# Kernel optimization log

Measured on AMD Instinct MI355X. Metric: run time of the kernel, lower is better.

## Reference

```python
import jax, jax.numpy as jnp
import numpy as np

N = 50000          # number of graph nodes
R = 4              # number of relation types (rt_num)
E = 800000         # edges per relation (avg degree 16)
D_IN = 128
D_OUT = 64
EPS = 1e-12        # torch F.normalize eps


def setup_inputs() -> dict:
    key = jax.random.key(0)
    k1, k2, k3, k4, k5 = jax.random.split(key, 5)
    x = jax.random.normal(k1, (N, D_IN), dtype=jnp.float32)
    W = jax.random.normal(k2, (R, D_IN, D_OUT), dtype=jnp.float32)
    b = jnp.zeros((R, D_OUT), dtype=jnp.float32)
    adj_vals = jax.random.uniform(k3, (R, E), dtype=jnp.float32)
    adj_rows = jax.random.randint(k4, (R, E), 0, N, dtype=jnp.int32)
    adj_cols = jax.random.randint(k5, (R, E), 0, N, dtype=jnp.int32)
    return {"x": x, "W": W, "b": b, "adj_vals": adj_vals,
            "adj_rows": adj_rows, "adj_cols": adj_cols, "dropout": 0}


def reference(x, W, b, adj_vals, adj_rows, adj_cols, dropout):
    # dropout == 0 -> F.dropout is the identity; reference is deterministic.
    # Per-relation dense projection: xw[r] = x @ W[r]   -> [R, N, D_OUT]
    xw = jnp.einsum('nd,rdo->rno', x, W)

    def per_relation(xw_r, rows_r, cols_r, vals_r, b_r):
        # sparse adjacency SpMM: out[i] = sum_e vals[e] * xw[cols[e]] for rows[e]==i
        msg = xw_r[cols_r] * vals_r[:, None]                  # [E, D_OUT] gather
        agg = jax.ops.segment_sum(msg, rows_r, num_segments=N)  # [N, D_OUT] scatter-add
        return jax.nn.relu(agg + b_r)                          # bias + act

    outs = jax.vmap(per_relation)(xw, adj_rows, adj_cols, adj_vals, b)  # [R, N, D_OUT]
    total = jnp.sum(outs, axis=0)                               # cross-relation sum
    # L2 normalize over feature dim (torch F.normalize, dim=1)
    norm = jnp.maximum(jnp.linalg.norm(total, axis=1, keepdims=True), EPS)
    return total / norm
```

## Files before the change

### kernel.cpp

```cpp
#include <hip/hip_runtime.h>
#include <hip/hip_bf16.h>
#include <stdint.h>

#define NN 50000
#define DI 128
#define DO 64
#define NE 800000
#define NR 4
#define NB 782
#define NBUCK (NR*NB)
#define PCHUNK 7168
#define PWG ((NE + PCHUNK - 1) / PCHUNK)
#define RSCAP 4096

typedef short short8 __attribute__((ext_vector_type(8)));
typedef float f32x4  __attribute__((ext_vector_type(4)));
union FragU { uint4 u; short8 s; };

__device__ __forceinline__ uint32_t bfb(float f)
{
    __hip_bfloat16 h = __float2bfloat16(f);
    return (uint32_t)*reinterpret_cast<unsigned short*>(&h);
}

template<int N, int PER, int BLK>
__device__ inline void block_exscan(int* a)
{
    __shared__ int wsum[BLK / 64];
    int tid = threadIdx.x;
    int base = tid * PER;
    int v[PER]; int s = 0;
    #pragma unroll
    for (int j = 0; j < PER; ++j) {
        int idx = base + j;
        int x = (idx < N) ? a[idx] : 0;
        v[j] = s; s += x;
    }
    int lane = tid & 63, wv = tid >> 6;
    int inc = s;
    #pragma unroll
    for (int off = 1; off < 64; off <<= 1) {
        int u = __shfl_up(inc, off);
        if (lane >= off) inc += u;
    }
    if (lane == 63) wsum[wv] = inc;
    __syncthreads();
    int woff = 0;
    for (int w = 0; w < wv; ++w) woff += wsum[w];
    int tb = woff + inc - s;
    #pragma unroll
    for (int j = 0; j < PER; ++j) {
        int idx = base + j;
        if (idx < N) a[idx] = tb + v[j];
    }
}

__global__ __launch_bounds__(256) void convx_kernel(
    const float* __restrict__ x, uint2* __restrict__ xb)
{
    int i = blockIdx.x * 256 + threadIdx.x;
    int stride = gridDim.x * 256;
    const int total = NN * DI / 4;
    const float4* x4 = (const float4*)x;
    for (; i < total; i += stride) {
        float4 v = x4[i];
        uint2 o;
        o.x = bfb(v.x) | (bfb(v.y) << 16);
        o.y = bfb(v.z) | (bfb(v.w) << 16);
        xb[i] = o;
    }
}

__global__ __launch_bounds__(256) void wtrans_kernel(
    const float* __restrict__ W, uint16_t* __restrict__ wt)
{
    int i = blockIdx.x * 256 + threadIdx.x;
    if (i >= NR * DI * DO) return;
    int r = i >> 13;
    int k = (i >> 6) & 127;
    int n = i & 63;
    wt[((size_t)(r * DO + n) << 7) + k] = (uint16_t)bfb(W[i]);
}

__global__ __launch_bounds__(256) void gemm_mfma_kernel(
    const uint4* __restrict__ xb4, const uint4* __restrict__ wt4,
    uint16_t* __restrict__ xwb)
{
    int tid = threadIdx.x;
    int wv = __builtin_amdgcn_readfirstlane(tid >> 6);
    int lane = tid & 63;
    int n0 = blockIdx.x * 64 + wv * 16;
    if (n0 >= NN) return;
    int m16 = lane & 15, g = lane >> 4;

    FragU a[4];
    #pragma unroll
    for (int ks = 0; ks < 4; ++ks)
        a[ks].u = xb4[(size_t)(n0 + m16) * 16 + ks * 4 + g];

    #pragma unroll
    for (int r = 0; r < NR; ++r) {
        #pragma unroll
        for (int ct = 0; ct < 4; ++ct) {
            f32x4 acc = {0.f, 0.f, 0.f, 0.f};
            #pragma unroll
            for (int ks = 0; ks < 4; ++ks) {
                FragU b;
                b.u = wt4[(size_t)((r * DO + ct * 16 + m16) * 16) + ks * 4 + g];
                acc = __builtin_amdgcn_mfma_f32_16x16x32_bf16(
                    a[ks].s, b.s, acc, 0, 0, 0);
            }
            #pragma unroll
            for (int j = 0; j < 4; ++j) {
                int m = g * 4 + j;
                xwb[((size_t)r * NN + n0 + m) * 64 + ct * 16 + m16] =
                    (uint16_t)bfb(acc[j]);
            }
        }
    }
}

__global__ __launch_bounds__(256) void gemm_kernel(
    const float* __restrict__ x, const float* __restrict__ W,
    __hip_bfloat16* __restrict__ xwb)
{
    __shared__ float Wl[DI * DO];
    for (int i = threadIdx.x; i < DI * DO; i += 256) Wl[i] = W[i];
    __syncthreads();

    int wv   = __builtin_amdgcn_readfirstlane((int)(threadIdx.x >> 6));
    int lane = threadIdx.x & 63;
    int n0   = blockIdx.x * 32 + wv * 8;
    if (n0 >= NN) return;
    int nrows = NN - n0; if (nrows > 8) nrows = 8;

    if (nrows == 8) {
        const float* xr = x + (size_t)n0 * DI;
        float acc[8] = {0.f,0.f,0.f,0.f,0.f,0.f,0.f,0.f};
        #pragma unroll 8
        for (int k = 0; k < DI; ++k) {
            float w = Wl[k * DO + lane];
            #pragma unroll
            for (int rr = 0; rr < 8; ++rr)
                acc[rr] = fmaf(xr[(size_t)rr * DI + k], w, acc[rr]);
        }
        #pragma unroll
        for (int rr = 0; rr < 8; ++rr)
            xwb[(size_t)(n0 + rr) * DO + lane] = __float2bfloat16(acc[rr]);
    } else {
        for (int rr = 0; rr < nrows; ++rr) {
            const float* xr = x + (size_t)(n0 + rr) * DI;
            float acc = 0.f;
            for (int k = 0; k < DI; ++k)
                acc = fmaf(xr[k], Wl[k * DO + lane], acc);
            xwb[(size_t)(n0 + rr) * DO + lane] = __float2bfloat16(acc);
        }
    }
}

__global__ __launch_bounds__(256) void bhist_kernel(
    const int* __restrict__ rows, int* __restrict__ gtot)
{
    __shared__ int h[NB];
    int r = blockIdx.y;
    int tid = threadIdx.x;
    for (int i = tid; i < NB; i += 256) h[i] = 0;
    __syncthreads();
    const int4* rr4 = (const int4*)(rows + (size_t)r * NE);
    for (int k = blockIdx.x * 256 + tid; k < NE / 4; k += gridDim.x * 256) {
        int4 v = rr4[k];
        atomicAdd(&h[v.x >> 6], 1);
        atomicAdd(&h[v.y >> 6], 1);
        atomicAdd(&h[v.z >> 6], 1);
        atomicAdd(&h[v.w >> 6], 1);
    }
    __syncthreads();
    int* gt = gtot + r * NB;
    for (int i = tid; i < NB; i += 256)
        if (h[i]) atomicAdd(&gt[i], h[i]);
}

__global__ __launch_bounds__(512) void bases_kernel(
    const int* __restrict__ gtot, int* __restrict__ gstart,
    int* __restrict__ gcur)
{
    __shared__ int a[NBUCK + 1];
    int tid = threadIdx.x;
    for (int i = tid; i < NBUCK + 1; i += 512) a[i] = (i < NBUCK) ? gtot[i] : 0;
    __syncthreads();
    block_exscan<NBUCK + 1, 7, 512>(a);
    __syncthreads();
    for (int i = tid; i < NBUCK + 1; i += 512) {
        gstart[i] = a[i];
        if (i < NBUCK) gcur[i] = a[i];
    }
}

__global__ __launch_bounds__(512) void place_kernel(
    const int* __restrict__ rows, const int* __restrict__ cols,
    const float* __restrict__ vals, int* __restrict__ gcur,
    int2* __restrict__ csr)
{
    __shared__ int lofs[NB + 1];
    __shared__ int gbase[NB];
    __shared__ int2 stag[PCHUNK];
    int r = blockIdx.y;
    int tid = threadIdx.x;
    int e0 = blockIdx.x * PCHUNK;
    int cnt = NE - e0; if (cnt > PCHUNK) cnt = PCHUNK;
    const int*   rr = rows + (size_t)r * NE + e0;
    const int*   cc = cols + (size_t)r * NE + e0;
    const float* vv = vals + (size_t)r * NE + e0;

    for (int i = tid; i <= NB; i += 512) lofs[i] = 0;
    __syncthreads();
    for (int k = tid; k < cnt; k += 512) atomicAdd(&lofs[rr[k] >> 6], 1);
    __syncthreads();
    block_exscan<NB + 1, 2, 512>(lofs);
    __syncthreads();
    for (int b = tid; b < NB; b += 512) {
        int c = lofs[b + 1] - lofs[b];
        if (c > 0) gbase[b] = atomicAdd(&gcur[r * NB + b], c);
    }
    __syncthreads();
    for (int k = tid; k < cnt; k += 512) {
        int row = rr[k];
        int b = row >> 6;
        int slot = atomicAdd(&lofs[b], 1);
        stag[slot] = make_int2((cc[k] & 0xFFFF) | ((row & 63) << 16) | (b << 22),
                               __float_as_int(vv[k]));
    }
    __syncthreads();
    for (int i = tid; i < cnt; i += 512) {
        int2 t = stag[i];
        unsigned b2 = ((unsigned)t.x) >> 22;
        int start = b2 ? lofs[b2 - 1] : 0;
        csr[gbase[b2] + (i - start)] = t;
    }
}

__global__ __launch_bounds__(256) void rowsort_kernel(
    int2* __restrict__ csr, const int* __restrict__ gstart,
    int* __restrict__ rowptr)
{
    __shared__ int2 stag[RSCAP];
    __shared__ int cnt[64];
    __shared__ int ofs[64];
    int blk = blockIdx.x;
    int r   = blockIdx.y;
    int b   = r * NB + blk;
    int s = gstart[b], e = gstart[b + 1];
    int cntE = e - s; if (cntE > RSCAP) cntE = RSCAP;
    int tid = threadIdx.x;
    if (tid < 64) cnt[tid] = 0;
    __syncthreads();

    int2 ed[RSCAP / 256];
    #pragma unroll
    for (int j = 0; j < RSCAP / 256; ++j) {
        int i = tid + j * 256;
        if (i < cntE) {
            ed[j] = csr[s + i];
            atomicAdd(&cnt[(ed[j].x >> 16) & 63], 1);
        }
    }
    __syncthreads();
    if (tid < 64) {
        int c = cnt[tid];
        int inc = c;
        #pragma unroll
        for (int off = 1; off < 64; off <<= 1) {
            int u = __shfl_up(inc, off);
            if (tid >= off) inc += u;
        }
        ofs[tid] = inc - c;
        int n = blk * 64 + tid;
        if (n < NN) rowptr[(size_t)r * NN + n] = s + inc - c;
        if (b == NBUCK - 1 && tid == 0)
            rowptr[(size_t)NR * NN] = gstart[NBUCK];
    }
    __syncthreads();
    #pragma unroll
    for (int j = 0; j < RSCAP / 256; ++j) {
        int i = tid + j * 256;
        if (i < cntE) {
            int rl = (ed[j].x >> 16) & 63;
            int slot = atomicAdd(&ofs[rl], 1);
            stag[slot] = ed[j];
        }
    }
    __syncthreads();
    for (int i = tid; i < cntE; i += 256) {
        int2 t = stag[i];
        t.x = (r * NN + (t.x & 0xFFFF)) << 4;
        csr[s + i] = t;
    }
}

struct Stage {
    float v[NR];
    uint2 u[NR];
};

__device__ __forceinline__ void stage_issue(
    int k, const int* deg, const int* ofsv, const float* valv,
    const uint2* __restrict__ xw2, int e4, int fq, Stage& st)
{
    #pragma unroll
    for (int r = 0; r < NR; ++r) {
        if (k < deg[r]) {
            int e = k + e4;
            bool valid = e < deg[r];
            int ec = valid ? e : 0;
            int ofs  = __shfl(ofsv[r], ec);
            float vv = __shfl(valv[r], ec);
            st.v[r] = valid ? vv : 0.f;
            st.u[r] = xw2[ofs + fq];
        } else {
            st.v[r] = 0.f;
            st.u[r] = make_uint2(0u, 0u);
        }
    }
}

__device__ __forceinline__ void stage_consume(const Stage& st, float a[NR][4])
{
    #pragma unroll
    for (int r = 0; r < NR; ++r) {
        float v = st.v[r];
        a[r][0] = fmaf(v, __uint_as_float(st.u[r].x << 16),          a[r][0]);
        a[r][1] = fmaf(v, __uint_as_float(st.u[r].x & 0xFFFF0000u),  a[r][1]);
        a[r][2] = fmaf(v, __uint_as_float(st.u[r].y << 16),          a[r][2]);
        a[r][3] = fmaf(v, __uint_as_float(st.u[r].y & 0xFFFF0000u),  a[r][3]);
    }
}

__global__ __launch_bounds__(256) void spmm_fused_kernel(
    const uint2* __restrict__ xw2, const int2* __restrict__ csr,
    const int* __restrict__ rowptr, const float* __restrict__ bias,
    float* __restrict__ out)
{
    int n = __builtin_amdgcn_readfirstlane(
        (int)((blockIdx.x * 256 + threadIdx.x) >> 6));
    int lane = threadIdx.x & 63;
    int e4 = lane >> 4, fq = lane & 15;
    if (n >= NN) return;

    int deg[NR]; int ofsv[NR]; float valv[NR];
    int sbeg[NR], send[NR];
    int maxdeg = 0;
    #pragma unroll
    for (int r = 0; r < NR; ++r) {
        sbeg[r] = rowptr[(size_t)r * NN + n];
        send[r] = rowptr[(size_t)r * NN + n + 1];
        int d = send[r] - sbeg[r];
        if (d > 64) d = 64;
        deg[r] = d;
        int2 cv = (lane < d) ? csr[sbeg[r] + lane] : make_int2(0, 0);
        ofsv[r] = cv.x;
        valv[r] = __int_as_float(cv.y);
        maxdeg = max(maxdeg, d);
    }

    float a[NR][4];
    #pragma unroll
    for (int r = 0; r < NR; ++r)
        #pragma unroll
        for (int j = 0; j < 4; ++j) a[r][j] = 0.f;

    Stage A, B;
    stage_issue(0, deg, ofsv, valv, xw2, e4, fq, A);
    for (int k = 0; k < maxdeg; k += 8) {
        stage_issue(k + 4, deg, ofsv, valv, xw2, e4, fq, B);
        stage_consume(A, a);
        stage_issue(k + 8, deg, ofsv, valv, xw2, e4, fq, A);
        stage_consume(B, a);
    }

    #pragma unroll
    for (int r = 0; r < NR; ++r) {
        for (int i = sbeg[r] + 64; i < send[r]; ++i) {
            int2 cv = csr[i];
            float v = (lane < 16) ? __int_as_float(cv.y) : 0.f;
            uint2 u = xw2[cv.x + fq];
            a[r][0] = fmaf(v, __uint_as_float(u.x << 16),         a[r][0]);
            a[r][1] = fmaf(v, __uint_as_float(u.x & 0xFFFF0000u), a[r][1]);
            a[r][2] = fmaf(v, __uint_as_float(u.y << 16),         a[r][2]);
            a[r][3] = fmaf(v, __uint_as_float(u.y & 0xFFFF0000u), a[r][3]);
        }
    }

    float t[4] = {0.f, 0.f, 0.f, 0.f};
    #pragma unroll
    for (int r = 0; r < NR; ++r) {
        #pragma unroll
        for (int j = 0; j < 4; ++j) {
            a[r][j] += __shfl_xor(a[r][j], 16);
            a[r][j] += __shfl_xor(a[r][j], 32);
        }
        float4 br = *(const float4*)&bias[r * DO + 4 * fq];
        t[0] += fmaxf(a[r][0] + br.x, 0.f);
        t[1] += fmaxf(a[r][1] + br.y, 0.f);
        t[2] += fmaxf(a[r][2] + br.z, 0.f);
        t[3] += fmaxf(a[r][3] + br.w, 0.f);
    }
    float s2 = t[0]*t[0] + t[1]*t[1] + t[2]*t[2] + t[3]*t[3];
    #pragma unroll
    for (int off = 8; off >= 1; off >>= 1) s2 += __shfl_xor(s2, off);
    float inv = 1.0f / fmaxf(sqrtf(s2), 1e-12f);
    if (lane < 16) {
        float4 o = make_float4(t[0]*inv, t[1]*inv, t[2]*inv, t[3]*inv);
        *(float4*)&out[(size_t)n * DO + 4 * fq] = o;
    }
}

__global__ __launch_bounds__(256) void scatter_kernel(
    const __hip_bfloat16* __restrict__ xwb, const float* __restrict__ vals,
    const int* __restrict__ rows, const int* __restrict__ cols,
    float* __restrict__ agg)
{
    const int nPairs = NE / 2;
    int gwave  = (blockIdx.x * 256 + threadIdx.x) >> 6;
    int half   = (threadIdx.x >> 5) & 1;
    int l32    = threadIdx.x & 31;
    int stride = gridDim.x * 4;
    const uint16_t* xw16 = reinterpret_cast<const uint16_t*>(xwb);
    for (int p = gwave; p < nPairs; p += stride) {
        int e = 2 * p + half;
        int row = rows[e]; int col = cols[e]; float v = vals[e];
        uint32_t packed = *reinterpret_cast<const uint32_t*>(
            xw16 + ((size_t)col << 6) + 2 * l32);
        float f0 = __uint_as_float(packed << 16);
        float f1 = __uint_as_float(packed & 0xFFFF0000u);
        float* dst = agg + ((size_t)row << 6) + 2 * l32;
        atomicAdd(dst,     v * f0);
        atomicAdd(dst + 1, v * f1);
    }
}

__global__ __launch_bounds__(256) void accum_kernel(
    float* __restrict__ agg, const float* __restrict__ b,
    float* __restrict__ out, int first)
{
    int i = blockIdx.x * 256 + threadIdx.x;
    if (i >= NN * DO) return;
    float v = agg[i] + b[i & (DO - 1)];
    agg[i] = 0.f;
    v = fmaxf(v, 0.f);
    out[i] = first ? v : (out[i] + v);
}

__global__ __launch_bounds__(256) void norm_kernel(float* __restrict__ out)
{
    int n = (blockIdx.x * 256 + threadIdx.x) >> 6;
    int lane = threadIdx.x & 63;
    if (n >= NN) return;
    size_t idx = (size_t)n * DO + lane;
    float t = out[idx];
    float s = t * t;
    #pragma unroll
    for (int off = 32; off >= 1; off >>= 1) s += __shfl_xor(s, off);
    out[idx] = t / fmaxf(sqrtf(s), 1e-12f);
}

extern "C" void kernel_launch(void* const* d_in, const int* in_sizes, int n_in,
                              void* d_out, int out_size, void* d_ws, size_t ws_size,
                              hipStream_t stream)
{
    const float* x    = (const float*)d_in[0];
    const float* W    = (const float*)d_in[1];
    const float* b    = (const float*)d_in[2];
    const float* vals = (const float*)d_in[3];
    const int*   rows = (const int*)d_in[4];
    const int*   cols = (const int*)d_in[5];
    float* out = (float*)d_out;
    char* ws = (char*)d_ws;

    const size_t O_XW = 0;
    const size_t O_CS = O_XW + (size_t)NR * NN * DO * 2;
    const size_t O_RP = O_CS + (size_t)NR * NE * 8;
    const size_t O_GT = O_RP + ((size_t)NR * NN + 4) * 4;
    const size_t O_GS = O_GT + (size_t)NBUCK * 4;
    const size_t O_GC = O_GS + (size_t)(NBUCK + 1) * 4;
    const size_t NEED = O_GC + (size_t)NBUCK * 4;
    const size_t O_XB = O_CS;
    const size_t O_WT = O_CS + 13u * 1024 * 1024;

    if (ws_size >= NEED) {
        __hip_bfloat16* xwb = (__hip_bfloat16*)(ws + O_XW);
        int2* csr   = (int2*)(ws + O_CS);
        int* rowptr = (int*)(ws + O_RP);
        int* gtot   = (int*)(ws + O_GT);
        int* gstart = (int*)(ws + O_GS);
        int* gcur   = (int*)(ws + O_GC);
        uint2* xb   = (uint2*)(ws + O_XB);
        uint16_t* wt = (uint16_t*)(ws + O_WT);

        hipMemsetAsync(gtot, 0, (size_t)NBUCK * 4, stream);
        convx_kernel<<<dim3(2048), dim3(256), 0, stream>>>(x, xb);
        wtrans_kernel<<<dim3(128), dim3(256), 0, stream>>>(W, wt);
        gemm_mfma_kernel<<<dim3(NB), dim3(256), 0, stream>>>(
            (const uint4*)xb, (const uint4*)wt, (uint16_t*)xwb);
        bhist_kernel<<<dim3(32, NR), dim3(256), 0, stream>>>(rows, gtot);
        bases_kernel<<<dim3(1), dim3(512), 0, stream>>>(gtot, gstart, gcur);
        place_kernel<<<dim3(PWG, NR), dim3(512), 0, stream>>>(rows, cols, vals, gcur, csr);
        rowsort_kernel<<<dim3(NB, NR), dim3(256), 0, stream>>>(csr, gstart, rowptr);
        spmm_fused_kernel<<<dim3((NN * 64 + 255) / 256), dim3(256), 0, stream>>>(
            (const uint2*)xwb, csr, rowptr, b, out);
    } else {
        __hip_bfloat16* xwb = (__hip_bfloat16*)ws;
        float* agg = (float*)(ws + (size_t)NN * DO * 2);
        hipMemsetAsync(agg, 0, (size_t)NN * DO * 4, stream);
        for (int r = 0; r < NR; ++r) {
            gemm_kernel<<<dim3((NN + 31) / 32), dim3(256), 0, stream>>>(
                x, W + (size_t)r * DI * DO, xwb);
            scatter_kernel<<<dim3(2048), dim3(256), 0, stream>>>(
                xwb, vals + (size_t)r * NE, rows + (size_t)r * NE,
                cols + (size_t)r * NE, agg);
            accum_kernel<<<dim3((NN * DO + 255) / 256), dim3(256), 0, stream>>>(
                agg, b + (size_t)r * DO, out, r == 0);
        }
        norm_kernel<<<dim3((NN * DO + 255) / 256), dim3(256), 0, stream>>>(out);
    }
}
```

Baseline: 188.8 us.

## Merge prep kernels and fold bucket scan into LDS-staged MFMA GEMM

Combines the x conversion, W transpose and row histogram into one launch partitioned by block index, and folds the bucket exclusive scan into an extra block of the GEMM kernel. This removes three kernel launches and the gaps between them. The GEMM now works on 128 rows per block and stages results in LDS so each relation's output is written with coalesced 16-byte stores. The SpMM stage loop also drops its per-lane validity select and pads degrees to a multiple of 4, which relies on the zeroed CSR loads for lanes past the true degree.

```diff
diff --git a/kernel.cpp b/kernel.cpp
--- a/kernel.cpp
+++ b/kernel.cpp
@@ -12,6 +12,8 @@
 #define PCHUNK 7168
 #define PWG ((NE + PCHUNK - 1) / PCHUNK)
 #define RSCAP 4096
+#define CONVB 1024
+#define GEMMB ((NN + 127) / 128)
 
 typedef short short8 __attribute__((ext_vector_type(8)));
 typedef float f32x4  __attribute__((ext_vector_type(4)));
@@ -55,68 +57,329 @@
     }
 }
 
-__global__ __launch_bounds__(256) void convx_kernel(
-    const float* __restrict__ x, uint2* __restrict__ xb)
-{
-    int i = blockIdx.x * 256 + threadIdx.x;
-    int stride = gridDim.x * 256;
-    const int total = NN * DI / 4;
-    const float4* x4 = (const float4*)x;
-    for (; i < total; i += stride) {
-        float4 v = x4[i];
-        uint2 o;
-        o.x = bfb(v.x) | (bfb(v.y) << 16);
-        o.y = bfb(v.z) | (bfb(v.w) << 16);
-        xb[i] = o;
-    }
-}
-
-__global__ __launch_bounds__(256) void wtrans_kernel(
-    const float* __restrict__ W, uint16_t* __restrict__ wt)
-{
-    int i = blockIdx.x * 256 + threadIdx.x;
-    if (i >= NR * DI * DO) return;
-    int r = i >> 13;
-    int k = (i >> 6) & 127;
-    int n = i & 63;
-    wt[((size_t)(r * DO + n) << 7) + k] = (uint16_t)bfb(W[i]);
-}
-
-__global__ __launch_bounds__(256) void gemm_mfma_kernel(
+__global__ __launch_bounds__(256) void prep_kernel(
+    const float* __restrict__ x, const float* __restrict__ W,
+    const int* __restrict__ rows,
+    uint2* __restrict__ xb, uint16_t* __restrict__ wt,
+    int* __restrict__ gtot)
+{
+    __shared__ int h[NB];
+    int bid = blockIdx.x, tid = threadIdx.x;
+
+    if (bid < CONVB) {
+        const int total = NN * DI / 4;
+        const float4* x4 = (const float4*)x;
+        for (int i = bid * 256 + tid; i < total; i += CONVB * 256) {
+            float4 v = x4[i];
+            uint2 o;
+            o.x = bfb(v.x) | (bfb(v.y) << 16);
+            o.y = bfb(v.z) | (bfb(v.w) << 16);
+            xb[i] = o;
+        }
+    } else if (bid < CONVB + 128) {
+        int i = (bid - CONVB) * 256 + tid;
+        int r = i >> 13;
+        int k = (i >> 6) & 127;
+        int n = i & 63;
+        wt[((size_t)(r * DO + n) << 7) + k] = (uint16_t)bfb(W[i]);
+    } else {
+        int bb = bid - (CONVB + 128);
+        int r = bb >> 5, sub = bb & 31;
+        for (int i = tid; i < NB; i += 256) h[i] = 0;
+        __syncthreads();
+        const int4* rr4 = (const int4*)(rows + (size_t)r * NE);
+        for (int k = sub * 256 + tid; k < NE / 4; k += 32 * 256) {
+            int4 v = rr4[k];
+            atomicAdd(&h[v.x >> 6], 1);
+            atomicAdd(&h[v.y >> 6], 1);
+            atomicAdd(&h[v.z >> 6], 1);
+            atomicAdd(&h[v.w >> 6], 1);
+        }
+        __syncthreads();
+        int* gt = gtot + r * NB;
+        for (int i = tid; i < NB; i += 256)
+            if (h[i]) atomicAdd(&gt[i], h[i]);
+    }
+}
+
+__global__ __launch_bounds__(512) void gemm_bases_kernel(
     const uint4* __restrict__ xb4, const uint4* __restrict__ wt4,
-    uint16_t* __restrict__ xwb)
-{
+    uint16_t* __restrict__ xwb,
+    const int* __restrict__ gtot, int* __restrict__ gstart,
+    int* __restrict__ gcur)
+{
+    __shared__ __align__(16) uint16_t tile[128 * 64];
+    __shared__ int a[NBUCK + 1];
     int tid = threadIdx.x;
+
+    if (blockIdx.x == GEMMB) {
+        for (int i = tid; i < NBUCK + 1; i += 512)
+            a[i] = (i < NBUCK) ? gtot[i] : 0;
+        __syncthreads();
+        block_exscan<NBUCK + 1, 7, 512>(a);
+        __syncthreads();
+        for (int i = tid; i < NBUCK + 1; i += 512) {
+            gstart[i] = a[i];
+            if (i < NBUCK) gcur[i] = a[i];
+        }
+        return;
+    }
+
     int wv = __builtin_amdgcn_readfirstlane(tid >> 6);
     int lane = tid & 63;
-    int n0 = blockIdx.x * 64 + wv * 16;
-    if (n0 >= NN) return;
+    int n0 = blockIdx.x * 128 + wv * 16;
     int m16 = lane & 15, g = lane >> 4;
-
-    FragU a[4];
-    #pragma unroll
-    for (int ks = 0; ks < 4; ++ks)
-        a[ks].u = xb4[(size_t)(n0 + m16) * 16 + ks * 4 + g];
-
+    bool act = (n0 < NN);
+
+    FragU af[4];
+    if (act) {
+        #pragma unroll
+        for (int ks = 0; ks < 4; ++ks)
+            af[ks].u = xb4[(size_t)(n0 + m16) * 16 + ks * 4 + g];
+    }
+
+    int rows = NN - blockIdx.x * 128; if (rows > 128) rows = 128;
+
+    for (int r = 0; r < NR; ++r) {
+        if (act) {
+            #pragma unroll
+            for (int ct = 0; ct < 4; ++ct) {
+                f32x4 acc = {0.f, 0.f, 0.f, 0.f};
+                #pragma unroll
+                for (int ks = 0; ks < 4; ++ks) {
+                    FragU b;
+                    b.u = wt4[(size_t)((r * DO + ct * 16 + m16) * 16) + ks * 4 + g];
+                    acc = __builtin_amdgcn_mfma_f32_16x16x32_bf16(
+                        af[ks].s, b.s, acc, 0, 0, 0);
+                }
+                #pragma unroll
+                for (int j = 0; j < 4; ++j)
+                    tile[(wv * 16 + g * 4 + j) * 64 + ct * 16 + m16] =
+                        (uint16_t)bfb(acc[j]);
+            }
+        }
+        __syncthreads();
+        uint4* dst = (uint4*)(xwb + ((size_t)r * NN + blockIdx.x * 128) * 64);
+        int tot = rows * 8;
+        for (int i = tid; i < tot; i += 512)
+            dst[i] = ((const uint4*)tile)[i];
+        __syncthreads();
+    }
+}
+
+__global__ __launch_bounds__(512) void place_kernel(
+    const int* __restrict__ rows, const int* __restrict__ cols,
+    const float* __restrict__ vals, int* __restrict__ gcur,
+    int2* __restrict__ csr)
+{
+    __shared__ int lofs[NB + 1];
+    __shared__ int gbase[NB];
+    __shared__ int2 stag[PCHUNK];
+    int r = blockIdx.y;
+    int tid = threadIdx.x;
+    int e0 = blockIdx.x * PCHUNK;
+    int cnt = NE - e0; if (cnt > PCHUNK) cnt = PCHUNK;
+    const int*   rr = rows + (size_t)r * NE + e0;
+    const int*   cc = cols + (size_t)r * NE + e0;
+    const float* vv = vals + (size_t)r * NE + e0;
+
+    for (int i = tid; i <= NB; i += 512) lofs[i] = 0;
+    __syncthreads();
+    for (int k = tid; k < cnt; k += 512) atomicAdd(&lofs[rr[k] >> 6], 1);
+    __syncthreads();
+    block_exscan<NB + 1, 2, 512>(lofs);
+    __syncthreads();
+    for (int b = tid; b < NB; b += 512) {
+        int c = lofs[b + 1] - lofs[b];
+        if (c > 0) gbase[b] = atomicAdd(&gcur[r * NB + b], c);
+    }
+    __syncthreads();
+    for (int k = tid; k < cnt; k += 512) {
+        int row = rr[k];
+        int b = row >> 6;
+        int slot = atomicAdd(&lofs[b], 1);
+        stag[slot] = make_int2((cc[k] & 0xFFFF) | ((row & 63) << 16) | (b << 22),
+                               __float_as_int(vv[k]));
+    }
+    __syncthreads();
+    for (int i = tid; i < cnt; i += 512) {
+        int2 t = stag[i];
+        unsigned b2 = ((unsigned)t.x) >> 22;
+        int start = b2 ? lofs[b2 - 1] : 0;
+        csr[gbase[b2] + (i - start)] = t;
+    }
+}
+
+__global__ __launch_bounds__(256) void rowsort_kernel(
+    int2* __restrict__ csr, const int* __restrict__ gstart,
+    int* __restrict__ rowptr)
+{
+    __shared__ int2 stag[RSCAP];
+    __shared__ int cnt[64];
+    __shared__ int ofs[64];
+    int blk = blockIdx.x;
+    int r   = blockIdx.y;
+    int b   = r * NB + blk;
+    int s = gstart[b], e = gstart[b + 1];
+    int cntE = e - s; if (cntE > RSCAP) cntE = RSCAP;
+    int tid = threadIdx.x;
+    if (tid < 64) cnt[tid] = 0;
+    __syncthreads();
+
+    int2 ed[RSCAP / 256];
+    #pragma unroll
+    for (int j = 0; j < RSCAP / 256; ++j) {
+        int i = tid + j * 256;
+        if (i < cntE) {
+            ed[j] = csr[s + i];
+            atomicAdd(&cnt[(ed[j].x >> 16) & 63], 1);
+        }
+    }
+    __syncthreads();
+    if (tid < 64) {
+        int c = cnt[tid];
+        int inc = c;
+        #pragma unroll
+        for (int off = 1; off < 64; off <<= 1) {
+            int u = __shfl_up(inc, off);
+            if (tid >= off) inc += u;
+        }
+        ofs[tid] = inc - c;
+        int n = blk * 64 + tid;
+        if (n < NN) rowptr[(size_t)r * NN + n] = s + inc - c;
+        if (b == NBUCK - 1 && tid == 0)
+            rowptr[(size_t)NR * NN] = gstart[NBUCK];
+    }
+    __syncthreads();
+    #pragma unroll
+    for (int j = 0; j < RSCAP / 256; ++j) {
+        int i = tid + j * 256;
+        if (i < cntE) {
+            int rl = (ed[j].x >> 16) & 63;
+            int slot = atomicAdd(&ofs[rl], 1);
+            stag[slot] = ed[j];
+        }
+    }
+    __syncthreads();
+    for (int i = tid; i < cntE; i += 256) {
+        int2 t = stag[i];
+        t.x = (r * NN + (t.x & 0xFFFF)) << 4;
+        csr[s + i] = t;
+    }
+}
+
+struct Stage {
+    float v[NR];
+    uint2 u[NR];
+};
+
+__device__ __forceinline__ void stage_issue(
+    int k, const int* dege, const int* ofsv, const float* valv,
+    const uint2* __restrict__ xw2, int e4, int fq, Stage& st)
+{
+    #pragma unroll
+    for (int r = 0; r < NR; ++r) {
+        if (k < dege[r]) {
+            int ec = k + e4;
+            int ofs  = __shfl(ofsv[r], ec);
+            float vv = __shfl(valv[r], ec);
+            st.v[r] = vv;
+            st.u[r] = xw2[ofs + fq];
+        } else {
+            st.v[r] = 0.f;
+            st.u[r] = make_uint2(0u, 0u);
+        }
+    }
+}
+
+__device__ __forceinline__ void stage_consume(const Stage& st, float a[NR][4])
+{
+    #pragma unroll
+    for (int r = 0; r < NR; ++r) {
+        float v = st.v[r];
+        a[r][0] = fmaf(v, __uint_as_float(st.u[r].x << 16),          a[r][0]);
+        a[r][1] = fmaf(v, __uint_as_float(st.u[r].x & 0xFFFF0000u),  a[r][1]);
+        a[r][2] = fmaf(v, __uint_as_float(st.u[r].y << 16),          a[r][2]);
+        a[r][3] = fmaf(v, __uint_as_float(st.u[r].y & 0xFFFF0000u),  a[r][3]);
+    }
+}
+
+__global__ __launch_bounds__(256) void spmm_fused_kernel(
+    const uint2* __restrict__ xw2, const int2* __restrict__ csr,
+    const int* __restrict__ rowptr, const float* __restrict__ bias,
+    float* __restrict__ out)
+{
+    int n = __builtin_amdgcn_readfirstlane(
+        (int)((blockIdx.x * 256 + threadIdx.x) >> 6));
+    int lane = threadIdx.x & 63;
+    int e4 = lane >> 4, fq = lane & 15;
+    if (n >= NN) return;
+
+    int dege[NR]; int ofsv[NR]; float valv[NR];
+    int sbeg[NR], send[NR];
+    int maxdeg = 0;
+    #pragma unroll
+    for (int r = 0; r < NR; ++r) {
+        sbeg[r] = rowptr[(size_t)r * NN + n];
+        send[r] = rowptr[(size_t)r * NN + n + 1];
+        int d = send[r] - sbeg[r];
+        if (d > 64) d = 64;
+        int2 cv = (lane < d) ? csr[sbeg[r] + lane] : make_int2(0, 0);
+        ofsv[r] = cv.x;
+        valv[r] = __int_as_float(cv.y);
+        dege[r] = (d + 3) & ~3;
+        maxdeg = max(maxdeg, dege[r]);
+    }
+
+    float a[NR][4];
+    #pragma unroll
+    for (int r = 0; r < NR; ++r)
+        #pragma unroll
+        for (int j = 0; j < 4; ++j) a[r][j] = 0.f;
+
+    Stage A, B;
+    stage_issue(0, dege, ofsv, valv, xw2, e4, fq, A);
+    for (int k = 0; k < maxdeg; k += 8) {
+        stage_issue(k + 4, dege, ofsv, valv, xw2, e4, fq, B);
+        stage_consume(A, a);
+        stage_issue(k + 8, dege, ofsv, valv, xw2, e4, fq, A);
+        stage_consume(B, a);
+    }
+
+    #pragma unroll
+    for (int r = 0; r < NR; ++r) {
+        for (int i = sbeg[r] + 64; i < send[r]; ++i) {
+            int2 cv = csr[i];
+            float v = (lane < 16) ? __int_as_float(cv.y) : 0.f;
+            uint2 u = xw2[cv.x + fq];
+            a[r][0] = fmaf(v, __uint_as_float(u.x << 16),         a[r][0]);
+            a[r][1] = fmaf(v, __uint_as_float(u.x & 0xFFFF0000u), a[r][1]);
+            a[r][2] = fmaf(v, __uint_as_float(u.y << 16),         a[r][2]);
+            a[r][3] = fmaf(v, __uint_as_float(u.y & 0xFFFF0000u), a[r][3]);
+        }
+    }
+
+    float t[4] = {0.f, 0.f, 0.f, 0.f};
     #pragma unroll
     for (int r = 0; r < NR; ++r) {
         #pragma unroll
-        for (int ct = 0; ct < 4; ++ct) {
-            f32x4 acc = {0.f, 0.f, 0.f, 0.f};
-            #pragma unroll
-            for (int ks = 0; ks < 4; ++ks) {
-                FragU b;
-                b.u = wt4[(size_t)((r * DO + ct * 16 + m16) * 16) + ks * 4 + g];
-                acc = __builtin_amdgcn_mfma_f32_16x16x32_bf16(
-                    a[ks].s, b.s, acc, 0, 0, 0);
-            }
-            #pragma unroll
-            for (int j = 0; j < 4; ++j) {
-                int m = g * 4 + j;
-                xwb[((size_t)r * NN + n0 + m) * 64 + ct * 16 + m16] =
-                    (uint16_t)bfb(acc[j]);
-            }
-        }
+        for (int j = 0; j < 4; ++j) {
+            a[r][j] += __shfl_xor(a[r][j], 16);
+            a[r][j] += __shfl_xor(a[r][j], 32);
+        }
+        float4 br = *(const float4*)&bias[r * DO + 4 * fq];
+        t[0] += fmaxf(a[r][0] + br.x, 0.f);
+        t[1] += fmaxf(a[r][1] + br.y, 0.f);
+        t[2] += fmaxf(a[r][2] + br.z, 0.f);
+        t[3] += fmaxf(a[r][3] + br.w, 0.f);
+    }
+    float s2 = t[0]*t[0] + t[1]*t[1] + t[2]*t[2] + t[3]*t[3];
+    #pragma unroll
+    for (int off = 8; off >= 1; off >>= 1) s2 += __shfl_xor(s2, off);
+    float inv = 1.0f / fmaxf(sqrtf(s2), 1e-12f);
+    if (lane < 16) {
+        float4 o = make_float4(t[0]*inv, t[1]*inv, t[2]*inv, t[3]*inv);
+        *(float4*)&out[(size_t)n * DO + 4 * fq] = o;
     }
 }
 
@@ -155,262 +418,6 @@
                 acc = fmaf(xr[k], Wl[k * DO + lane], acc);
             xwb[(size_t)(n0 + rr) * DO + lane] = __float2bfloat16(acc);
         }
-    }
-}
-
-__global__ __launch_bounds__(256) void bhist_kernel(
-    const int* __restrict__ rows, int* __restrict__ gtot)
-{
-    __shared__ int h[NB];
-    int r = blockIdx.y;
-    int tid = threadIdx.x;
-    for (int i = tid; i < NB; i += 256) h[i] = 0;
-    __syncthreads();
-    const int4* rr4 = (const int4*)(rows + (size_t)r * NE);
-    for (int k = blockIdx.x * 256 + tid; k < NE / 4; k += gridDim.x * 256) {
-        int4 v = rr4[k];
-        atomicAdd(&h[v.x >> 6], 1);
-        atomicAdd(&h[v.y >> 6], 1);
-        atomicAdd(&h[v.z >> 6], 1);
-        atomicAdd(&h[v.w >> 6], 1);
-    }
-    __syncthreads();
-    int* gt = gtot + r * NB;
-    for (int i = tid; i < NB; i += 256)
-        if (h[i]) atomicAdd(&gt[i], h[i]);
-}
-
-__global__ __launch_bounds__(512) void bases_kernel(
-    const int* __restrict__ gtot, int* __restrict__ gstart,
-    int* __restrict__ gcur)
-{
-    __shared__ int a[NBUCK + 1];
-    int tid = threadIdx.x;
-    for (int i = tid; i < NBUCK + 1; i += 512) a[i] = (i < NBUCK) ? gtot[i] : 0;
-    __syncthreads();
-    block_exscan<NBUCK + 1, 7, 512>(a);
-    __syncthreads();
-    for (int i = tid; i < NBUCK + 1; i += 512) {
-        gstart[i] = a[i];
-        if (i < NBUCK) gcur[i] = a[i];
-    }
-}
-
-__global__ __launch_bounds__(512) void place_kernel(
-    const int* __restrict__ rows, const int* __restrict__ cols,
-    const float* __restrict__ vals, int* __restrict__ gcur,
-    int2* __restrict__ csr)
-{
-    __shared__ int lofs[NB + 1];
-    __shared__ int gbase[NB];
-    __shared__ int2 stag[PCHUNK];
-    int r = blockIdx.y;
-    int tid = threadIdx.x;
-    int e0 = blockIdx.x * PCHUNK;
-    int cnt = NE - e0; if (cnt > PCHUNK) cnt = PCHUNK;
-    const int*   rr = rows + (size_t)r * NE + e0;
-    const int*   cc = cols + (size_t)r * NE + e0;
-    const float* vv = vals + (size_t)r * NE + e0;
-
-    for (int i = tid; i <= NB; i += 512) lofs[i] = 0;
-    __syncthreads();
-    for (int k = tid; k < cnt; k += 512) atomicAdd(&lofs[rr[k] >> 6], 1);
-    __syncthreads();
-    block_exscan<NB + 1, 2, 512>(lofs);
-    __syncthreads();
-    for (int b = tid; b < NB; b += 512) {
-        int c = lofs[b + 1] - lofs[b];
-        if (c > 0) gbase[b] = atomicAdd(&gcur[r * NB + b], c);
-    }
-    __syncthreads();
-    for (int k = tid; k < cnt; k += 512) {
-        int row = rr[k];
-        int b = row >> 6;
-        int slot = atomicAdd(&lofs[b], 1);
-        stag[slot] = make_int2((cc[k] & 0xFFFF) | ((row & 63) << 16) | (b << 22),
-                               __float_as_int(vv[k]));
-    }
-    __syncthreads();
-    for (int i = tid; i < cnt; i += 512) {
-        int2 t = stag[i];
-        unsigned b2 = ((unsigned)t.x) >> 22;
-        int start = b2 ? lofs[b2 - 1] : 0;
-        csr[gbase[b2] + (i - start)] = t;
-    }
-}
-
-__global__ __launch_bounds__(256) void rowsort_kernel(
-    int2* __restrict__ csr, const int* __restrict__ gstart,
-    int* __restrict__ rowptr)
-{
-    __shared__ int2 stag[RSCAP];
-    __shared__ int cnt[64];
-    __shared__ int ofs[64];
-    int blk = blockIdx.x;
-    int r   = blockIdx.y;
-    int b   = r * NB + blk;
-    int s = gstart[b], e = gstart[b + 1];
-    int cntE = e - s; if (cntE > RSCAP) cntE = RSCAP;
-    int tid = threadIdx.x;
-    if (tid < 64) cnt[tid] = 0;
-    __syncthreads();
-
-    int2 ed[RSCAP / 256];
-    #pragma unroll
-    for (int j = 0; j < RSCAP / 256; ++j) {
-        int i = tid + j * 256;
-        if (i < cntE) {
-            ed[j] = csr[s + i];
-            atomicAdd(&cnt[(ed[j].x >> 16) & 63], 1);
-        }
-    }
-    __syncthreads();
-    if (tid < 64) {
-        int c = cnt[tid];
-        int inc = c;
-        #pragma unroll
-        for (int off = 1; off < 64; off <<= 1) {
-            int u = __shfl_up(inc, off);
-            if (tid >= off) inc += u;
-        }
-        ofs[tid] = inc - c;
-        int n = blk * 64 + tid;
-        if (n < NN) rowptr[(size_t)r * NN + n] = s + inc - c;
-        if (b == NBUCK - 1 && tid == 0)
-            rowptr[(size_t)NR * NN] = gstart[NBUCK];
-    }
-    __syncthreads();
-    #pragma unroll
-    for (int j = 0; j < RSCAP / 256; ++j) {
-        int i = tid + j * 256;
-        if (i < cntE) {
-            int rl = (ed[j].x >> 16) & 63;
-            int slot = atomicAdd(&ofs[rl], 1);
-            stag[slot] = ed[j];
-        }
-    }
-    __syncthreads();
-    for (int i = tid; i < cntE; i += 256) {
-        int2 t = stag[i];
-        t.x = (r * NN + (t.x & 0xFFFF)) << 4;
-        csr[s + i] = t;
-    }
-}
-
-struct Stage {
-    float v[NR];
-    uint2 u[NR];
-};
-
-__device__ __forceinline__ void stage_issue(
-    int k, const int* deg, const int* ofsv, const float* valv,
-    const uint2* __restrict__ xw2, int e4, int fq, Stage& st)
-{
-    #pragma unroll
-    for (int r = 0; r < NR; ++r) {
-        if (k < deg[r]) {
-            int e = k + e4;
-            bool valid = e < deg[r];
-            int ec = valid ? e : 0;
-            int ofs  = __shfl(ofsv[r], ec);
-            float vv = __shfl(valv[r], ec);
-            st.v[r] = valid ? vv : 0.f;
-            st.u[r] = xw2[ofs + fq];
-        } else {
-            st.v[r] = 0.f;
-            st.u[r] = make_uint2(0u, 0u);
-        }
-    }
-}
-
-__device__ __forceinline__ void stage_consume(const Stage& st, float a[NR][4])
-{
-    #pragma unroll
-    for (int r = 0; r < NR; ++r) {
-        float v = st.v[r];
-        a[r][0] = fmaf(v, __uint_as_float(st.u[r].x << 16),          a[r][0]);
-        a[r][1] = fmaf(v, __uint_as_float(st.u[r].x & 0xFFFF0000u),  a[r][1]);
-        a[r][2] = fmaf(v, __uint_as_float(st.u[r].y << 16),          a[r][2]);
-        a[r][3] = fmaf(v, __uint_as_float(st.u[r].y & 0xFFFF0000u),  a[r][3]);
-    }
-}
-
-__global__ __launch_bounds__(256) void spmm_fused_kernel(
-    const uint2* __restrict__ xw2, const int2* __restrict__ csr,
-    const int* __restrict__ rowptr, const float* __restrict__ bias,
-    float* __restrict__ out)
-{
-    int n = __builtin_amdgcn_readfirstlane(
-        (int)((blockIdx.x * 256 + threadIdx.x) >> 6));
-    int lane = threadIdx.x & 63;
-    int e4 = lane >> 4, fq = lane & 15;
-    if (n >= NN) return;
-
-    int deg[NR]; int ofsv[NR]; float valv[NR];
-    int sbeg[NR], send[NR];
-    int maxdeg = 0;
-    #pragma unroll
-    for (int r = 0; r < NR; ++r) {
-        sbeg[r] = rowptr[(size_t)r * NN + n];
-        send[r] = rowptr[(size_t)r * NN + n + 1];
-        int d = send[r] - sbeg[r];
-        if (d > 64) d = 64;
-        deg[r] = d;
-        int2 cv = (lane < d) ? csr[sbeg[r] + lane] : make_int2(0, 0);
-        ofsv[r] = cv.x;
-        valv[r] = __int_as_float(cv.y);
-        maxdeg = max(maxdeg, d);
-    }
-
-    float a[NR][4];
-    #pragma unroll
-    for (int r = 0; r < NR; ++r)
-        #pragma unroll
-        for (int j = 0; j < 4; ++j) a[r][j] = 0.f;
-
-    Stage A, B;
-    stage_issue(0, deg, ofsv, valv, xw2, e4, fq, A);
-    for (int k = 0; k < maxdeg; k += 8) {
-        stage_issue(k + 4, deg, ofsv, valv, xw2, e4, fq, B);
-        stage_consume(A, a);
-        stage_issue(k + 8, deg, ofsv, valv, xw2, e4, fq, A);
-        stage_consume(B, a);
-    }
-
-    #pragma unroll
-    for (int r = 0; r < NR; ++r) {
-        for (int i = sbeg[r] + 64; i < send[r]; ++i) {
-            int2 cv = csr[i];
-            float v = (lane < 16) ? __int_as_float(cv.y) : 0.f;
-            uint2 u = xw2[cv.x + fq];
-            a[r][0] = fmaf(v, __uint_as_float(u.x << 16),         a[r][0]);
-            a[r][1] = fmaf(v, __uint_as_float(u.x & 0xFFFF0000u), a[r][1]);
-            a[r][2] = fmaf(v, __uint_as_float(u.y << 16),         a[r][2]);
-            a[r][3] = fmaf(v, __uint_as_float(u.y & 0xFFFF0000u), a[r][3]);
-        }
-    }
-
-    float t[4] = {0.f, 0.f, 0.f, 0.f};
-    #pragma unroll
-    for (int r = 0; r < NR; ++r) {
-        #pragma unroll
-        for (int j = 0; j < 4; ++j) {
-            a[r][j] += __shfl_xor(a[r][j], 16);
-            a[r][j] += __shfl_xor(a[r][j], 32);
-        }
-        float4 br = *(const float4*)&bias[r * DO + 4 * fq];
-        t[0] += fmaxf(a[r][0] + br.x, 0.f);
-        t[1] += fmaxf(a[r][1] + br.y, 0.f);
-        t[2] += fmaxf(a[r][2] + br.z, 0.f);
-        t[3] += fmaxf(a[r][3] + br.w, 0.f);
-    }
-    float s2 = t[0]*t[0] + t[1]*t[1] + t[2]*t[2] + t[3]*t[3];
-    #pragma unroll
-    for (int off = 8; off >= 1; off >>= 1) s2 += __shfl_xor(s2, off);
-    float inv = 1.0f / fmaxf(sqrtf(s2), 1e-12f);
-    if (lane < 16) {
-        float4 o = make_float4(t[0]*inv, t[1]*inv, t[2]*inv, t[3]*inv);
-        *(float4*)&out[(size_t)n * DO + 4 * fq] = o;
     }
 }
 
@@ -497,13 +504,13 @@
         uint16_t* wt = (uint16_t*)(ws + O_WT);
 
         hipMemsetAsync(gtot, 0, (size_t)NBUCK * 4, stream);
-        convx_kernel<<<dim3(2048), dim3(256), 0, stream>>>(x, xb);
-        wtrans_kernel<<<dim3(128), dim3(256), 0, stream>>>(W, wt);
-        gemm_mfma_kernel<<<dim3(NB), dim3(256), 0, stream>>>(
-            (const uint4*)xb, (const uint4*)wt, (uint16_t*)xwb);
-        bhist_kernel<<<dim3(32, NR), dim3(256), 0, stream>>>(rows, gtot);
-        bases_kernel<<<dim3(1), dim3(512), 0, stream>>>(gtot, gstart, gcur);
-        place_kernel<<<dim3(PWG, NR), dim3(512), 0, stream>>>(rows, cols, vals, gcur, csr);
+        prep_kernel<<<dim3(CONVB + 128 + 128), dim3(256), 0, stream>>>(
+            x, W, rows, xb, wt, gtot);
+        gemm_bases_kernel<<<dim3(GEMMB + 1), dim3(512), 0, stream>>>(
+            (const uint4*)xb, (const uint4*)wt, (uint16_t*)xwb,
+            gtot, gstart, gcur);
+        place_kernel<<<dim3(PWG, NR), dim3(512), 0, stream>>>(
+            rows, cols, vals, gcur, csr);
         rowsort_kernel<<<dim3(NB, NR), dim3(256), 0, stream>>>(csr, gstart, rowptr);
         spmm_fused_kernel<<<dim3((NN * 64 + 255) / 256), dim3(256), 0, stream>>>(
             (const uint2*)xwb, csr, rowptr, b, out);
```

Result: faster. 178.6 us (-5.4%).
